# Optimization experiments

Measured on AMD Instinct MI355X. Metric: run time of the kernel, lower is better.

## Reference

```python
import jax, jax.numpy as jnp
import numpy as np

N = 262144          # nodes
F_NODE, F_EDGE = 64, 16
OUT = [64, 64, 64]  # hidden sizes per layer / readout fingerprint size
TARGET = 12
N_DEG = 4           # d = [1,2,3,4]
IN0 = F_NODE + F_EDGE   # duvenaud message out size, layer 0
IN1 = OUT[0] + F_EDGE   # layer 1


def _build_graph():
    # ring: (i, i+1 mod N) -> every node degree 2
    ring = np.stack([np.arange(N), (np.arange(N) + 1) % N], 1)
    # chords: (2i, 2i + N//2) for i < N//8 -> distinct endpoints, bumps degree to 3
    i = np.arange(N // 8)
    chords = np.stack([2 * i, 2 * i + N // 2], 1)
    und = np.concatenate([ring, chords], 0)            # [E, 2] undirected edges
    E = und.shape[0]
    # directed (both directions) for message passing
    src = np.concatenate([und[:, 0], und[:, 1]]).astype(np.int64)
    dst = np.concatenate([und[:, 1], und[:, 0]]).astype(np.int64)
    eid = np.concatenate([np.arange(E), np.arange(E)]).astype(np.int64)
    deg = np.bincount(np.concatenate([und[:, 0], und[:, 1]]), minlength=N)
    deg_idx = (deg - 1).astype(np.int64)               # index into d=[1,2,3,4]
    return src, dst, eid, deg_idx, E


def setup_inputs() -> dict:
    key = jax.random.key(0)
    ks = jax.random.split(key, 9)
    src, dst, eid, deg_idx, E = _build_graph()
    s0 = 1.0 / np.sqrt(IN0)
    sR = 1.0 / np.sqrt(OUT[0])
    return {
        "h_in": jax.random.normal(ks[0], (N, F_NODE), jnp.float32),
        "edge_feat": jax.random.normal(ks[1], (E, F_EDGE), jnp.float32),
        "U0": jax.random.normal(ks[2], (N_DEG, IN0, OUT[0]), jnp.float32) * s0,
        "U1": jax.random.normal(ks[3], (N_DEG, IN1, OUT[1]), jnp.float32) * s0,
        "R0": jax.random.normal(ks[4], (F_NODE, OUT[2]), jnp.float32) * sR,
        "R1": jax.random.normal(ks[5], (OUT[0], OUT[2]), jnp.float32) * sR,
        "R2": jax.random.normal(ks[6], (OUT[1], OUT[2]), jnp.float32) * sR,
        "W_out": jax.random.normal(ks[7], (OUT[2], TARGET), jnp.float32) * sR,
        "b_out": jax.random.normal(ks[8], (TARGET,), jnp.float32) * 0.01,
        "edge_src": jnp.asarray(src),
        "edge_dst": jnp.asarray(dst),
        "edge_eid": jnp.asarray(eid),
        "deg_idx": jnp.asarray(deg_idx),
    }


def reference(h_in, edge_feat, U0, U1, R0, R1, R2, W_out, b_out,
              edge_src, edge_dst, edge_eid, deg_idx):
    ef = edge_feat[edge_eid]  # [2E, F_EDGE] directed-edge features

    def step(h, U):
        # duvenaud message: m_{v<-w} = concat(h_w, e_vw); sum over neighbors
        m = jnp.concatenate([h[edge_src], ef], axis=1)              # [2E, in]
        m_agg = jax.ops.segment_sum(m, edge_dst, num_segments=N)    # [N, in]
        # duvenaud update: h_v' = sigmoid(W_{deg(v)} m_v)
        out_all = jnp.einsum('ni,dio->ndo', m_agg, U)               # [N, D, out]
        sel = jnp.take_along_axis(out_all, deg_idx[:, None, None], axis=1)[:, 0, :]
        return jax.nn.sigmoid(sel)

    h1 = step(h_in, U0)
    h2 = step(h1, U1)
    # duvenaud readout: sum over layers & nodes of softmax(h_l @ R_l), then linear
    fp = (jax.nn.softmax(h_in @ R0, axis=-1)
          + jax.nn.softmax(h1 @ R1, axis=-1)
          + jax.nn.softmax(h2 @ R2, axis=-1)).sum(axis=0)           # [OUT[2]]
    return fp @ W_out + b_out                                       # [TARGET]
```

## Files before the change

kernel.cpp:

```cpp
#include <hip/hip_runtime.h>
#include <stdint.h>

#define NN 262144
#define VMASK (NN - 1)
#define GRID_BLKS (NN / 128)

typedef __attribute__((ext_vector_type(8))) short short8;
typedef __attribute__((ext_vector_type(4))) float f32x4;

__device__ __forceinline__ float bf2f(uint16_t h) {
    union { uint32_t u; float f; } a; a.u = ((uint32_t)h) << 16; return a.f;
}
__device__ __forceinline__ uint16_t f2bf(float x) {
    union { float f; uint32_t u; } a; a.f = x;
    uint32_t r = a.u + 0x7fffu + ((a.u >> 16) & 1u);
    return (uint16_t)(r >> 16);
}
__device__ __forceinline__ float sigm(float x) { return 1.f / (1.f + __expf(-x)); }

__device__ __forceinline__ void chord_of(int v, int& cn, int& ce) {
    cn = -1; ce = -1;
    if ((v & 1) == 0) {
        if (v < NN / 4)                            { cn = v + NN / 2; ce = NN + (v >> 1); }
        else if (v >= NN / 2 && v < (3 * NN) / 4)  { cn = v - NN / 2; ce = NN + ((v - NN / 2) >> 1); }
    }
}

__global__ void prep_weights(const float* __restrict__ U0, const float* __restrict__ U1,
                             const float* __restrict__ R0, const float* __restrict__ R1,
                             const float* __restrict__ R2,
                             uint16_t* __restrict__ Ut0, uint16_t* __restrict__ Ut1,
                             uint16_t* __restrict__ Rt)
{
    int idx = blockIdx.x * 256 + threadIdx.x;
    if (idx < 10240) {
        int o = idx / 160, k = idx - o * 160;
        float v = (k < 80) ? U0[5120 + k * 64 + o] : U0[2 * 5120 + (k - 80) * 64 + o];
        Ut0[o * 160 + k] = f2bf(v);
    } else if (idx < 20480) {
        int r = idx - 10240;
        int o = r / 160, k = r - o * 160;
        float v = (k < 80) ? U1[5120 + k * 64 + o] : U1[2 * 5120 + (k - 80) * 64 + o];
        Ut1[o * 160 + k] = f2bf(v);
    } else if (idx < 20480 + 3 * 4096) {
        int r = idx - 20480;
        int layer = r >> 12;
        int e = r & 4095;
        int o = e >> 6, i = e & 63;
        const float* R = (layer == 0) ? R0 : ((layer == 1) ? R1 : R2);
        Rt[layer * 4096 + o * 64 + i] = f2bf(R[i * 64 + o]);
    }
}

template<int MODE>
__device__ __forceinline__ void build_afr(const float* __restrict__ hf,
                                          const uint16_t* __restrict__ hb,
                                          const float* __restrict__ ef,
                                          int v, int koff, short8* afr)
{
    const int vm1 = (v - 1) & VMASK, vp1 = (v + 1) & VMASK;
    const int e1 = vm1;
    int cn, ce; chord_of(v, cn, ce);
    const int off = (cn >= 0) ? 80 : 0;
    const short8 zz = {0, 0, 0, 0, 0, 0, 0, 0};
#pragma unroll
    for (int ks = 0; ks < 5; ++ks) {
        const int mk = ks * 32 + koff - off;
        short8 r = zz;
        if (mk >= 0 && mk < 64) {
            float s[8];
            if (MODE == 0) {
                const float4* x4 = (const float4*)(hf + (size_t)vm1 * 64 + mk);
                const float4* y4 = (const float4*)(hf + (size_t)vp1 * 64 + mk);
                float4 x0 = x4[0], x1 = x4[1], y0 = y4[0], y1 = y4[1];
                s[0] = x0.x + y0.x; s[1] = x0.y + y0.y; s[2] = x0.z + y0.z; s[3] = x0.w + y0.w;
                s[4] = x1.x + y1.x; s[5] = x1.y + y1.y; s[6] = x1.z + y1.z; s[7] = x1.w + y1.w;
                if (cn >= 0) {
                    const float4* z4 = (const float4*)(hf + (size_t)cn * 64 + mk);
                    float4 z0 = z4[0], z1 = z4[1];
                    s[0] += z0.x; s[1] += z0.y; s[2] += z0.z; s[3] += z0.w;
                    s[4] += z1.x; s[5] += z1.y; s[6] += z1.z; s[7] += z1.w;
                }
            } else {
                short8 x = *(const short8*)(hb + (size_t)vm1 * 64 + mk);
                short8 y = *(const short8*)(hb + (size_t)vp1 * 64 + mk);
#pragma unroll
                for (int j = 0; j < 8; ++j) s[j] = bf2f((uint16_t)x[j]) + bf2f((uint16_t)y[j]);
                if (cn >= 0) {
                    short8 zv = *(const short8*)(hb + (size_t)cn * 64 + mk);
#pragma unroll
                    for (int j = 0; j < 8; ++j) s[j] += bf2f((uint16_t)zv[j]);
                }
            }
#pragma unroll
            for (int j = 0; j < 8; ++j) r[j] = (short)f2bf(s[j]);
        } else if (mk >= 64 && mk < 80) {
            const int ek = mk - 64;
            const float4* p4 = (const float4*)(ef + (size_t)e1 * 16 + ek);
            const float4* q4 = (const float4*)(ef + (size_t)v * 16 + ek);
            float4 p0 = p4[0], p1 = p4[1], q0 = q4[0], q1 = q4[1];
            float s[8] = { p0.x + q0.x, p0.y + q0.y, p0.z + q0.z, p0.w + q0.w,
                           p1.x + q1.x, p1.y + q1.y, p1.z + q1.z, p1.w + q1.w };
            if (ce >= 0) {
                const float4* c4 = (const float4*)(ef + (size_t)ce * 16 + ek);
                float4 c0 = c4[0], c1 = c4[1];
                s[0] += c0.x; s[1] += c0.y; s[2] += c0.z; s[3] += c0.w;
                s[4] += c1.x; s[5] += c1.y; s[6] += c1.z; s[7] += c1.w;
            }
#pragma unroll
            for (int j = 0; j < 8; ++j) r[j] = (short)f2bf(s[j]);
        }
        afr[ks] = r;
    }
}

__device__ __forceinline__ void softmax_acc(const f32x4& acc0, const f32x4& acc1,
                                            const f32x4& acc2, const f32x4& acc3,
                                            float& ca0, float& ca1, float& ca2, float& ca3)
{
#pragma unroll
    for (int r = 0; r < 4; ++r) {
        float z0 = acc0[r], z1 = acc1[r], z2 = acc2[r], z3 = acc3[r];
        float m = fmaxf(fmaxf(z0, z1), fmaxf(z2, z3));
        m = fmaxf(m, __shfl_xor(m, 1)); m = fmaxf(m, __shfl_xor(m, 2));
        m = fmaxf(m, __shfl_xor(m, 4)); m = fmaxf(m, __shfl_xor(m, 8));
        float e0 = __expf(z0 - m), e1 = __expf(z1 - m), e2 = __expf(z2 - m), e3 = __expf(z3 - m);
        float s = e0 + e1 + e2 + e3;
        s += __shfl_xor(s, 1); s += __shfl_xor(s, 2);
        s += __shfl_xor(s, 4); s += __shfl_xor(s, 8);
        const float inv = 1.f / s;
        ca0 += e0 * inv; ca1 += e1 * inv; ca2 += e2 * inv; ca3 += e3 * inv;
    }
}

template<int MODE>
__global__ __launch_bounds__(256, 4) void fused_layer(
    const float* __restrict__ hf, const uint16_t* __restrict__ hb,
    const float* __restrict__ ef,
    const uint16_t* __restrict__ Ut, const uint16_t* __restrict__ RtA,
    const uint16_t* __restrict__ Rt0, uint16_t* __restrict__ hout,
    float* __restrict__ fpacc)
{
    __shared__ alignas(16) uint16_t B[64][168];
    __shared__ alignas(16) uint16_t X[128][72];

    const int t = threadIdx.x, w = t >> 6, l = t & 63;
    const int bid = blockIdx.x;
    const int xcd = bid & 7, i = bid >> 3;
    const int chunk = ((i >> 7) << 10) | (xcd << 7) | (i & 127);
    const int vb = chunk * 128;
    const int row16 = l & 15, cq = l >> 4, koff = cq * 8;
    const int va = vb + w * 32 + row16;
    const int vbn = va + 16;

#pragma unroll
    for (int it = t; it < 1280; it += 256) {
        int o = it / 20, c = it - o * 20;
        *(short8*)&B[o][c * 8] = *(const short8*)(Ut + o * 160 + c * 8);
    }

    short8 afrA[5], afrB[5];
    build_afr<MODE>(hf, hb, ef, va,  koff, afrA);
    build_afr<MODE>(hf, hb, ef, vbn, koff, afrB);

    __syncthreads();

    const int bc = row16;
#pragma unroll
    for (int tile = 0; tile < 2; ++tile) {
        f32x4 acc0 = {0,0,0,0}, acc1 = {0,0,0,0}, acc2 = {0,0,0,0}, acc3 = {0,0,0,0};
#pragma unroll
        for (int ks = 0; ks < 5; ++ks) {
            const int kk = ks * 32 + koff;
            short8 a  = tile ? afrB[ks] : afrA[ks];
            short8 b0 = *(const short8*)&B[bc][kk];
            short8 b1 = *(const short8*)&B[16 + bc][kk];
            short8 b2 = *(const short8*)&B[32 + bc][kk];
            short8 b3 = *(const short8*)&B[48 + bc][kk];
            acc0 = __builtin_amdgcn_mfma_f32_16x16x32_bf16(a, b0, acc0, 0, 0, 0);
            acc1 = __builtin_amdgcn_mfma_f32_16x16x32_bf16(a, b1, acc1, 0, 0, 0);
            acc2 = __builtin_amdgcn_mfma_f32_16x16x32_bf16(a, b2, acc2, 0, 0, 0);
            acc3 = __builtin_amdgcn_mfma_f32_16x16x32_bf16(a, b3, acc3, 0, 0, 0);
        }
        const int row0 = w * 32 + tile * 16 + cq * 4;
#pragma unroll
        for (int r = 0; r < 4; ++r) {
            X[row0 + r][row16]      = f2bf(sigm(acc0[r]));
            X[row0 + r][16 + row16] = f2bf(sigm(acc1[r]));
            X[row0 + r][32 + row16] = f2bf(sigm(acc2[r]));
            X[row0 + r][48 + row16] = f2bf(sigm(acc3[r]));
        }
    }
    __syncthreads();

#pragma unroll
    for (int it = t; it < 512; it += 256) {
        int o = it >> 3, c = it & 7;
        *(short8*)&B[o][c * 8] = *(const short8*)(RtA + o * 64 + c * 8);
    }
    if (MODE == 0) {
#pragma unroll
        for (int it = t; it < 512; it += 256) {
            int o = it >> 3, c = it & 7;
            *(short8*)&B[o][72 + c * 8] = *(const short8*)(Rt0 + o * 64 + c * 8);
        }
#pragma unroll
        for (int it = t; it < 1024; it += 256) {
            int row = it >> 3, c = it & 7;
            *(short8*)(hout + (size_t)(vb + row) * 64 + c * 8) = *(const short8*)&X[row][c * 8];
        }
    }
    __syncthreads();

    short8 h0fa[2], h0fb[2];
    if (MODE == 0) {
#pragma unroll
        for (int tile = 0; tile < 2; ++tile) {
            const int v = tile ? vbn : va;
            const float4* s4 = (const float4*)(hf + (size_t)v * 64);
            float4 a0 = s4[cq * 2], a1 = s4[cq * 2 + 1];
            float4 b0 = s4[8 + cq * 2], b1 = s4[8 + cq * 2 + 1];
            short8 f0, f1;
            f0[0] = (short)f2bf(a0.x); f0[1] = (short)f2bf(a0.y);
            f0[2] = (short)f2bf(a0.z); f0[3] = (short)f2bf(a0.w);
            f0[4] = (short)f2bf(a1.x); f0[5] = (short)f2bf(a1.y);
            f0[6] = (short)f2bf(a1.z); f0[7] = (short)f2bf(a1.w);
            f1[0] = (short)f2bf(b0.x); f1[1] = (short)f2bf(b0.y);
            f1[2] = (short)f2bf(b0.z); f1[3] = (short)f2bf(b0.w);
            f1[4] = (short)f2bf(b1.x); f1[5] = (short)f2bf(b1.y);
            f1[6] = (short)f2bf(b1.z); f1[7] = (short)f2bf(b1.w);
            if (tile) { h0fb[0] = f0; h0fb[1] = f1; }
            else      { h0fa[0] = f0; h0fa[1] = f1; }
        }
    }

    float ca0 = 0.f, ca1 = 0.f, ca2 = 0.f, ca3 = 0.f;
#pragma unroll
    for (int tile = 0; tile < 2; ++tile) {
        const int ar = w * 32 + tile * 16 + row16;
        f32x4 acc0 = {0,0,0,0}, acc1 = {0,0,0,0}, acc2 = {0,0,0,0}, acc3 = {0,0,0,0};
#pragma unroll
        for (int ks = 0; ks < 2; ++ks) {
            const int kk = ks * 32 + koff;
            short8 a  = *(const short8*)&X[ar][kk];
            short8 b0 = *(const short8*)&B[bc][kk];
            short8 b1 = *(const short8*)&B[16 + bc][kk];
            short8 b2 = *(const short8*)&B[32 + bc][kk];
            short8 b3 = *(const short8*)&B[48 + bc][kk];
            acc0 = __builtin_amdgcn_mfma_f32_16x16x32_bf16(a, b0, acc0, 0, 0, 0);
            acc1 = __builtin_amdgcn_mfma_f32_16x16x32_bf16(a, b1, acc1, 0, 0, 0);
            acc2 = __builtin_amdgcn_mfma_f32_16x16x32_bf16(a, b2, acc2, 0, 0, 0);
            acc3 = __builtin_amdgcn_mfma_f32_16x16x32_bf16(a, b3, acc3, 0, 0, 0);
        }
        softmax_acc(acc0, acc1, acc2, acc3, ca0, ca1, ca2, ca3);
    }
    if (MODE == 0) {
#pragma unroll
        for (int tile = 0; tile < 2; ++tile) {
            f32x4 acc0 = {0,0,0,0}, acc1 = {0,0,0,0}, acc2 = {0,0,0,0}, acc3 = {0,0,0,0};
#pragma unroll
            for (int ks = 0; ks < 2; ++ks) {
                const int kk = ks * 32 + koff;
                short8 a  = tile ? h0fb[ks] : h0fa[ks];
                short8 b0 = *(const short8*)&B[bc][72 + kk];
                short8 b1 = *(const short8*)&B[16 + bc][72 + kk];
                short8 b2 = *(const short8*)&B[32 + bc][72 + kk];
                short8 b3 = *(const short8*)&B[48 + bc][72 + kk];
                acc0 = __builtin_amdgcn_mfma_f32_16x16x32_bf16(a, b0, acc0, 0, 0, 0);
                acc1 = __builtin_amdgcn_mfma_f32_16x16x32_bf16(a, b1, acc1, 0, 0, 0);
                acc2 = __builtin_amdgcn_mfma_f32_16x16x32_bf16(a, b2, acc2, 0, 0, 0);
                acc3 = __builtin_amdgcn_mfma_f32_16x16x32_bf16(a, b3, acc3, 0, 0, 0);
            }
            softmax_acc(acc0, acc1, acc2, acc3, ca0, ca1, ca2, ca3);
        }
    }

    ca0 += __shfl_xor(ca0, 16); ca0 += __shfl_xor(ca0, 32);
    ca1 += __shfl_xor(ca1, 16); ca1 += __shfl_xor(ca1, 32);
    ca2 += __shfl_xor(ca2, 16); ca2 += __shfl_xor(ca2, 32);
    ca3 += __shfl_xor(ca3, 16); ca3 += __shfl_xor(ca3, 32);
    __syncthreads();
    float* P = (float*)&X[0][0];
    if (cq == 0) {
        P[w * 64 + l]      = ca0;
        P[w * 64 + 16 + l] = ca1;
        P[w * 64 + 32 + l] = ca2;
        P[w * 64 + 48 + l] = ca3;
    }
    __syncthreads();
    if (t < 64)
        atomicAdd(&fpacc[(xcd << 6) + t], P[t] + P[64 + t] + P[128 + t] + P[192 + t]);
}

__global__ void final_kernel(const float* __restrict__ fpacc, const float* __restrict__ W,
                             const float* __restrict__ b, float* __restrict__ out)
{
    __shared__ float ft[64];
    const int t = threadIdx.x;
    if (t < 64) {
        float s = 0.f;
#pragma unroll
        for (int k = 0; k < 8; ++k) s += fpacc[k * 64 + t];
        ft[t] = s;
    }
    __syncthreads();
    if (t < 12) {
        float s = b[t];
#pragma unroll 8
        for (int j = 0; j < 64; ++j) s += ft[j] * W[j * 12 + t];
        out[t] = s;
    }
}

extern "C" void kernel_launch(void* const* d_in, const int* in_sizes, int n_in,
                              void* d_out, int out_size, void* d_ws, size_t ws_size,
                              hipStream_t stream)
{
    const float* h_in = (const float*)d_in[0];
    const float* ef   = (const float*)d_in[1];
    const float* U0   = (const float*)d_in[2];
    const float* U1   = (const float*)d_in[3];
    const float* R0   = (const float*)d_in[4];
    const float* R1   = (const float*)d_in[5];
    const float* R2   = (const float*)d_in[6];
    const float* W    = (const float*)d_in[7];
    const float* bo   = (const float*)d_in[8];

    uint16_t* h1  = (uint16_t*)d_ws;
    uint16_t* Ut0 = h1 + (size_t)NN * 64;
    uint16_t* Ut1 = Ut0 + 10240;
    uint16_t* Rt  = Ut1 + 10240;
    float* fpacc  = (float*)(Rt + 3 * 4096);

    hipMemsetAsync(fpacc, 0, 512 * sizeof(float), stream);

    prep_weights<<<128, 256, 0, stream>>>(U0, U1, R0, R1, R2, Ut0, Ut1, Rt);
    fused_layer<0><<<GRID_BLKS, 256, 0, stream>>>(h_in, nullptr, ef, Ut0,
                                                  Rt + 4096, Rt, h1, fpacc);
    fused_layer<1><<<GRID_BLKS, 256, 0, stream>>>(nullptr, h1, ef, Ut1,
                                                  Rt + 2 * 4096, nullptr, nullptr, fpacc);
    final_kernel<<<1, 64, 0, stream>>>(fpacc, W, bo, (float*)d_out);
}
```

Measured before the change: 113.3 us.

## Preload readout weights into dedicated LDS buffers and drop intermediate barriers

Readout weight matrices now get their own shared-memory buffers and are loaded at kernel start alongside the layer weights. This removes the mid-kernel reload and two of the block-wide barriers. After the layer GEMM, sigmoid outputs are staged per wave into an X tile that aliases the weight buffer. The readout GEMMs then read only their own wave's rows, so no further barrier is needed. The bf16 conversion switches to the library intrinsic and prep_weights launches more blocks. In exchange, LDS use per block rises and accumulator registers are held longer (TA array), which may lower occupancy.

```diff
diff --git a/kernel.cpp b/kernel.cpp
--- a/kernel.cpp
+++ b/kernel.cpp
@@ -1,4 +1,5 @@
 #include <hip/hip_runtime.h>
+#include <hip/hip_bf16.h>
 #include <stdint.h>
 
 #define NN 262144
@@ -12,9 +13,9 @@
     union { uint32_t u; float f; } a; a.u = ((uint32_t)h) << 16; return a.f;
 }
 __device__ __forceinline__ uint16_t f2bf(float x) {
-    union { float f; uint32_t u; } a; a.f = x;
-    uint32_t r = a.u + 0x7fffu + ((a.u >> 16) & 1u);
-    return (uint16_t)(r >> 16);
+    union { __hip_bfloat16 b; uint16_t u; } c;
+    c.b = __float2bfloat16(x);
+    return c.u;
 }
 __device__ __forceinline__ float sigm(float x) { return 1.f / (1.f + __expf(-x)); }
 
@@ -114,13 +115,13 @@
     }
 }
 
-__device__ __forceinline__ void softmax_acc(const f32x4& acc0, const f32x4& acc1,
-                                            const f32x4& acc2, const f32x4& acc3,
-                                            float& ca0, float& ca1, float& ca2, float& ca3)
+__device__ __forceinline__ void softmax_acc(const f32x4& a0, const f32x4& a1,
+                                            const f32x4& a2, const f32x4& a3,
+                                            float& c0, float& c1, float& c2, float& c3)
 {
 #pragma unroll
     for (int r = 0; r < 4; ++r) {
-        float z0 = acc0[r], z1 = acc1[r], z2 = acc2[r], z3 = acc3[r];
+        float z0 = a0[r], z1 = a1[r], z2 = a2[r], z3 = a3[r];
         float m = fmaxf(fmaxf(z0, z1), fmaxf(z2, z3));
         m = fmaxf(m, __shfl_xor(m, 1)); m = fmaxf(m, __shfl_xor(m, 2));
         m = fmaxf(m, __shfl_xor(m, 4)); m = fmaxf(m, __shfl_xor(m, 8));
@@ -129,20 +130,45 @@
         s += __shfl_xor(s, 1); s += __shfl_xor(s, 2);
         s += __shfl_xor(s, 4); s += __shfl_xor(s, 8);
         const float inv = 1.f / s;
-        ca0 += e0 * inv; ca1 += e1 * inv; ca2 += e2 * inv; ca3 += e3 * inv;
-    }
+        c0 += e0 * inv; c1 += e1 * inv; c2 += e2 * inv; c3 += e3 * inv;
+    }
+}
+
+__device__ __forceinline__ void ro_gemm(const uint16_t (*Rb)[68],
+                                        const short8& a0, const short8& a1,
+                                        int row16, int koff,
+                                        float& c0, float& c1, float& c2, float& c3)
+{
+    f32x4 q0 = {0,0,0,0}, q1 = {0,0,0,0}, q2 = {0,0,0,0}, q3 = {0,0,0,0};
+#pragma unroll
+    for (int ks = 0; ks < 2; ++ks) {
+        const int kk = ks * 32 + koff;
+        short8 a = ks ? a1 : a0;
+        short8 b0 = *(const short8*)&Rb[row16][kk];
+        short8 b1 = *(const short8*)&Rb[16 + row16][kk];
+        short8 b2 = *(const short8*)&Rb[32 + row16][kk];
+        short8 b3 = *(const short8*)&Rb[48 + row16][kk];
+        q0 = __builtin_amdgcn_mfma_f32_16x16x32_bf16(a, b0, q0, 0, 0, 0);
+        q1 = __builtin_amdgcn_mfma_f32_16x16x32_bf16(a, b1, q1, 0, 0, 0);
+        q2 = __builtin_amdgcn_mfma_f32_16x16x32_bf16(a, b2, q2, 0, 0, 0);
+        q3 = __builtin_amdgcn_mfma_f32_16x16x32_bf16(a, b3, q3, 0, 0, 0);
+    }
+    softmax_acc(q0, q1, q2, q3, c0, c1, c2, c3);
 }
 
 template<int MODE>
 __global__ __launch_bounds__(256, 4) void fused_layer(
     const float* __restrict__ hf, const uint16_t* __restrict__ hb,
     const float* __restrict__ ef,
-    const uint16_t* __restrict__ Ut, const uint16_t* __restrict__ RtA,
+    const uint16_t* __restrict__ Ug, const uint16_t* __restrict__ RtA,
     const uint16_t* __restrict__ Rt0, uint16_t* __restrict__ hout,
     float* __restrict__ fpacc)
 {
-    __shared__ alignas(16) uint16_t B[64][168];
-    __shared__ alignas(16) uint16_t X[128][72];
+    __shared__ alignas(16) uint16_t Bmem[64 * 168];
+    __shared__ alignas(16) uint16_t Rbuf[(MODE == 0 ? 2 : 1)][64][68];
+    __shared__ float P[256];
+    uint16_t (*Ut)[168] = (uint16_t(*)[168])Bmem;
+    uint16_t (*X)[76]   = (uint16_t(*)[76])Bmem;
 
     const int t = threadIdx.x, w = t >> 6, l = t & 63;
     const int bid = blockIdx.x;
@@ -156,7 +182,19 @@
 #pragma unroll
     for (int it = t; it < 1280; it += 256) {
         int o = it / 20, c = it - o * 20;
-        *(short8*)&B[o][c * 8] = *(const short8*)(Ut + o * 160 + c * 8);
+        *(short8*)&Ut[o][c * 8] = *(const short8*)(Ug + o * 160 + c * 8);
+    }
+#pragma unroll
+    for (int it = t; it < 512; it += 256) {
+        int o = it >> 3, c = it & 7;
+        *(short8*)&Rbuf[0][o][c * 8] = *(const short8*)(RtA + o * 64 + c * 8);
+    }
+    if (MODE == 0) {
+#pragma unroll
+        for (int it = t; it < 512; it += 256) {
+            int o = it >> 3, c = it & 7;
+            *(short8*)&Rbuf[1][o][c * 8] = *(const short8*)(Rt0 + o * 64 + c * 8);
+        }
     }
 
     short8 afrA[5], afrB[5];
@@ -166,6 +204,7 @@
     __syncthreads();
 
     const int bc = row16;
+    f32x4 TA[2][4];
 #pragma unroll
     for (int tile = 0; tile < 2; ++tile) {
         f32x4 acc0 = {0,0,0,0}, acc1 = {0,0,0,0}, acc2 = {0,0,0,0}, acc3 = {0,0,0,0};
@@ -173,46 +212,49 @@
         for (int ks = 0; ks < 5; ++ks) {
             const int kk = ks * 32 + koff;
             short8 a  = tile ? afrB[ks] : afrA[ks];
-            short8 b0 = *(const short8*)&B[bc][kk];
-            short8 b1 = *(const short8*)&B[16 + bc][kk];
-            short8 b2 = *(const short8*)&B[32 + bc][kk];
-            short8 b3 = *(const short8*)&B[48 + bc][kk];
+            short8 b0 = *(const short8*)&Ut[bc][kk];
+            short8 b1 = *(const short8*)&Ut[16 + bc][kk];
+            short8 b2 = *(const short8*)&Ut[32 + bc][kk];
+            short8 b3 = *(const short8*)&Ut[48 + bc][kk];
             acc0 = __builtin_amdgcn_mfma_f32_16x16x32_bf16(a, b0, acc0, 0, 0, 0);
             acc1 = __builtin_amdgcn_mfma_f32_16x16x32_bf16(a, b1, acc1, 0, 0, 0);
             acc2 = __builtin_amdgcn_mfma_f32_16x16x32_bf16(a, b2, acc2, 0, 0, 0);
             acc3 = __builtin_amdgcn_mfma_f32_16x16x32_bf16(a, b3, acc3, 0, 0, 0);
         }
+        TA[tile][0] = acc0; TA[tile][1] = acc1; TA[tile][2] = acc2; TA[tile][3] = acc3;
+    }
+
+    __syncthreads();
+
+#pragma unroll
+    for (int tile = 0; tile < 2; ++tile) {
         const int row0 = w * 32 + tile * 16 + cq * 4;
 #pragma unroll
         for (int r = 0; r < 4; ++r) {
-            X[row0 + r][row16]      = f2bf(sigm(acc0[r]));
-            X[row0 + r][16 + row16] = f2bf(sigm(acc1[r]));
-            X[row0 + r][32 + row16] = f2bf(sigm(acc2[r]));
-            X[row0 + r][48 + row16] = f2bf(sigm(acc3[r]));
-        }
-    }
-    __syncthreads();
-
-#pragma unroll
-    for (int it = t; it < 512; it += 256) {
-        int o = it >> 3, c = it & 7;
-        *(short8*)&B[o][c * 8] = *(const short8*)(RtA + o * 64 + c * 8);
-    }
+            X[row0 + r][row16]      = f2bf(sigm(TA[tile][0][r]));
+            X[row0 + r][16 + row16] = f2bf(sigm(TA[tile][1][r]));
+            X[row0 + r][32 + row16] = f2bf(sigm(TA[tile][2][r]));
+            X[row0 + r][48 + row16] = f2bf(sigm(TA[tile][3][r]));
+        }
+    }
+
     if (MODE == 0) {
 #pragma unroll
-        for (int it = t; it < 512; it += 256) {
-            int o = it >> 3, c = it & 7;
-            *(short8*)&B[o][72 + c * 8] = *(const short8*)(Rt0 + o * 64 + c * 8);
-        }
-#pragma unroll
-        for (int it = t; it < 1024; it += 256) {
-            int row = it >> 3, c = it & 7;
-            *(short8*)(hout + (size_t)(vb + row) * 64 + c * 8) = *(const short8*)&X[row][c * 8];
-        }
-    }
-    __syncthreads();
-
-    short8 h0fa[2], h0fb[2];
+        for (int it = l; it < 256; it += 64) {
+            int row = it >> 3, cc = it & 7;
+            *(short8*)(hout + ((size_t)vb + w * 32 + row) * 64 + cc * 8) =
+                *(const short8*)&X[w * 32 + row][cc * 8];
+        }
+    }
+
+    float ca0 = 0.f, ca1 = 0.f, ca2 = 0.f, ca3 = 0.f;
+#pragma unroll
+    for (int tile = 0; tile < 2; ++tile) {
+        const int ar = w * 32 + tile * 16 + row16;
+        short8 x0 = *(const short8*)&X[ar][koff];
+        short8 x1 = *(const short8*)&X[ar][32 + koff];
+        ro_gemm(Rbuf[0], x0, x1, row16, koff, ca0, ca1, ca2, ca3);
+    }
     if (MODE == 0) {
 #pragma unroll
         for (int tile = 0; tile < 2; ++tile) {
@@ -229,49 +271,7 @@
             f1[2] = (short)f2bf(b0.z); f1[3] = (short)f2bf(b0.w);
             f1[4] = (short)f2bf(b1.x); f1[5] = (short)f2bf(b1.y);
             f1[6] = (short)f2bf(b1.z); f1[7] = (short)f2bf(b1.w);
-            if (tile) { h0fb[0] = f0; h0fb[1] = f1; }
-            else      { h0fa[0] = f0; h0fa[1] = f1; }
-        }
-    }
-
-    float ca0 = 0.f, ca1 = 0.f, ca2 = 0.f, ca3 = 0.f;
-#pragma unroll
-    for (int tile = 0; tile < 2; ++tile) {
-        const int ar = w * 32 + tile * 16 + row16;
-        f32x4 acc0 = {0,0,0,0}, acc1 = {0,0,0,0}, acc2 = {0,0,0,0}, acc3 = {0,0,0,0};
-#pragma unroll
-        for (int ks = 0; ks < 2; ++ks) {
-            const int kk = ks * 32 + koff;
-            short8 a  = *(const short8*)&X[ar][kk];
-            short8 b0 = *(const short8*)&B[bc][kk];
-            short8 b1 = *(const short8*)&B[16 + bc][kk];
-            short8 b2 = *(const short8*)&B[32 + bc][kk];
-            short8 b3 = *(const short8*)&B[48 + bc][kk];
-            acc0 = __builtin_amdgcn_mfma_f32_16x16x32_bf16(a, b0, acc0, 0, 0, 0);
-            acc1 = __builtin_amdgcn_mfma_f32_16x16x32_bf16(a, b1, acc1, 0, 0, 0);
-            acc2 = __builtin_amdgcn_mfma_f32_16x16x32_bf16(a, b2, acc2, 0, 0, 0);
-            acc3 = __builtin_amdgcn_mfma_f32_16x16x32_bf16(a, b3, acc3, 0, 0, 0);
-        }
-        softmax_acc(acc0, acc1, acc2, acc3, ca0, ca1, ca2, ca3);
-    }
-    if (MODE == 0) {
-#pragma unroll
-        for (int tile = 0; tile < 2; ++tile) {
-            f32x4 acc0 = {0,0,0,0}, acc1 = {0,0,0,0}, acc2 = {0,0,0,0}, acc3 = {0,0,0,0};
-#pragma unroll
-            for (int ks = 0; ks < 2; ++ks) {
-                const int kk = ks * 32 + koff;
-                short8 a  = tile ? h0fb[ks] : h0fa[ks];
-                short8 b0 = *(const short8*)&B[bc][72 + kk];
-                short8 b1 = *(const short8*)&B[16 + bc][72 + kk];
-                short8 b2 = *(const short8*)&B[32 + bc][72 + kk];
-                short8 b3 = *(const short8*)&B[48 + bc][72 + kk];
-                acc0 = __builtin_amdgcn_mfma_f32_16x16x32_bf16(a, b0, acc0, 0, 0, 0);
-                acc1 = __builtin_amdgcn_mfma_f32_16x16x32_bf16(a, b1, acc1, 0, 0, 0);
-                acc2 = __builtin_amdgcn_mfma_f32_16x16x32_bf16(a, b2, acc2, 0, 0, 0);
-                acc3 = __builtin_amdgcn_mfma_f32_16x16x32_bf16(a, b3, acc3, 0, 0, 0);
-            }
-            softmax_acc(acc0, acc1, acc2, acc3, ca0, ca1, ca2, ca3);
+            ro_gemm(Rbuf[1], f0, f1, row16, koff, ca0, ca1, ca2, ca3);
         }
     }
 
@@ -279,8 +279,6 @@
     ca1 += __shfl_xor(ca1, 16); ca1 += __shfl_xor(ca1, 32);
     ca2 += __shfl_xor(ca2, 16); ca2 += __shfl_xor(ca2, 32);
     ca3 += __shfl_xor(ca3, 16); ca3 += __shfl_xor(ca3, 32);
-    __syncthreads();
-    float* P = (float*)&X[0][0];
     if (cq == 0) {
         P[w * 64 + l]      = ca0;
         P[w * 64 + 16 + l] = ca1;
@@ -330,11 +328,11 @@
     uint16_t* Ut0 = h1 + (size_t)NN * 64;
     uint16_t* Ut1 = Ut0 + 10240;
     uint16_t* Rt  = Ut1 + 10240;
-    float* fpacc  = (float*)(Rt + 3 * 4096);
+    float* fpacc  = (float*)(Rt + 12288);
 
     hipMemsetAsync(fpacc, 0, 512 * sizeof(float), stream);
 
-    prep_weights<<<128, 256, 0, stream>>>(U0, U1, R0, R1, R2, Ut0, Ut1, Rt);
+    prep_weights<<<144, 256, 0, stream>>>(U0, U1, R0, R1, R2, Ut0, Ut1, Rt);
     fused_layer<0><<<GRID_BLKS, 256, 0, stream>>>(h_in, nullptr, ef, Ut0,
                                                   Rt + 4096, Rt, h1, fpacc);
     fused_layer<1><<<GRID_BLKS, 256, 0, stream>>>(nullptr, h1, ef, Ut1,
```

Measured after the change: 135.0 us. +19.2%, slower.
